# Kernel tuning notes

Hardware: AMD Instinct MI355X
Metric: run time of the kernel (lower is better)

The kernel has to match this reference:

```python
import jax, jax.numpy as jnp
import numpy as np
from jax import lax

LENGTH, WIDTH = 64, 64
INPUT_DIM = 1


def _convlstm_layer(x_tbchw, W, b):
    """Run one ConvLSTM layer over time. x_tbchw: (L,B,Cin,H,W).
    W: (4*hid, Cin+hid, 3, 3), b: (4*hid,). Returns (outputs (L,B,hid,H,W), last_h)."""
    L, B, _, H, Wd = x_tbchw.shape
    hid = W.shape[0] // 4
    h0 = jnp.zeros((B, hid, H, Wd), dtype=x_tbchw.dtype)
    c0 = jnp.zeros((B, hid, H, Wd), dtype=x_tbchw.dtype)

    def step(carry, xt):
        h, c = carry
        z = lax.conv_general_dilated(
            jnp.concatenate([xt, h], axis=1), W,
            window_strides=(1, 1), padding='SAME',
            dimension_numbers=('NCHW', 'OIHW', 'NCHW'))
        z = z + b[None, :, None, None]
        cc_i, cc_f, cc_o, cc_g = jnp.split(z, 4, axis=1)
        c_next = jax.nn.sigmoid(cc_f) * c + jax.nn.sigmoid(cc_i) * jnp.tanh(cc_g)
        h_next = jax.nn.sigmoid(cc_o) * jnp.tanh(c_next)
        return (h_next, c_next), h_next

    (h_last, _), outs = lax.scan(step, (h0, c0), x_tbchw)
    return outs, h_last


def setup_inputs() -> dict:
    key = jax.random.key(0)
    k1, k2, k3 = jax.random.split(key, 3)
    B, L, N = 16, 12, LENGTH * WIDTH
    emd, out_len = 128, 12
    return {
        'history_data': jax.random.normal(k1, (B, L, N, 1), dtype=jnp.float32),
        'future_data': jnp.zeros((B, L, N, 1), dtype=jnp.float32),
        'W0': jax.random.normal(k2, (4 * emd, INPUT_DIM + emd, 3, 3), dtype=jnp.float32) * 0.05,
        'b0': jnp.zeros((4 * emd,), dtype=jnp.float32),
        'W1': jax.random.normal(k3, (4 * out_len, emd + out_len, 3, 3), dtype=jnp.float32) * 0.05,
        'b1': jnp.zeros((4 * out_len,), dtype=jnp.float32),
        'batch_seen': 0,
        'epoch': 0,
        'train': 1,
    }


def reference(history_data, future_data, W0, b0, W1, b1, batch_seen, epoch, train):
    B, L, N, C = history_data.shape
    # (B,L,1,H,W) -> (L,B,1,H,W) for time-major scan
    x = history_data[..., :INPUT_DIM].reshape(B, L, INPUT_DIM, LENGTH, WIDTH)
    x = jnp.transpose(x, (1, 0, 2, 3, 4))
    outs0, _ = _convlstm_layer(x, W0, b0)          # (L,B,emd,H,W)
    _, h_last = _convlstm_layer(outs0, W1, b1)     # (B,out_len,H,W)
    prediction = h_last.reshape(B, L, LENGTH * WIDTH)[..., None]  # (B,L,N,1)
    return prediction
```

## Files before the change

### kernel.cpp

```cpp
#include <hip/hip_runtime.h>
#include <hip/hip_bf16.h>


typedef __attribute__((ext_vector_type(8))) short short8;
typedef __attribute__((ext_vector_type(4))) float float4v;

#define CS 160
#define KT0 1152
#define KTOT 1440
#define RSTR 2112
#define BSTR4 8448
#define BSTR6 12672

__device__ __forceinline__ float sigf(float x) { return 1.f / (1.f + __expf(-x)); }
__device__ __forceinline__ short f2hs(float v) {
  _Float16 h = (_Float16)v;
  return *(short*)&h;
}
__device__ __forceinline__ float bs2f(short s) {
  __hip_bfloat16 h; *(short*)&h = s; return __bfloat162float(h);
}
__device__ __forceinline__ short f2bs(float v) {
  __hip_bfloat16 h = __float2bfloat16(v);
  return *(short*)&h;
}

__device__ __forceinline__ void async_ld16(const short* g, short* l) {
  __builtin_amdgcn_global_load_lds(
      (const __attribute__((address_space(1))) unsigned int*)g,
      (__attribute__((address_space(3))) unsigned int*)l, 16, 0, 0);
}

__device__ __forceinline__ void stage_one4(const short* __restrict__ rowPtr, bool rowOK,
                                           short* dstRow, int lane,
                                           const short* __restrict__ zp, int j) {
  int e = j * 64 + lane;
  int px = e >> 2, v = e & 3;
  int xx = px - 1;
  bool ok = rowOK && (xx >= 0);
  const short* g = ok ? (rowPtr + (size_t)xx * CS + v * 8) : zp;
  async_ld16(g, dstRow + e * 8);
}

__device__ __forceinline__ void stage_row4(const short* __restrict__ rowPtr, bool rowOK,
                                           short* dstRow, int lane,
                                           const short* __restrict__ zp) {
  #pragma unroll
  for (int j = 0; j < 4; ++j) stage_one4(rowPtr, rowOK, dstRow, lane, zp, j);
}

__device__ __forceinline__ short8 tail_load(const short* __restrict__ srcChunk,
                                            bool rowOK, int lane) {
  short8 tv = {0, 0, 0, 0, 0, 0, 0, 0};
  if (lane < 4 && rowOK) tv = *(const short8*)(srcChunk + (size_t)63 * CS + lane * 8);
  return tv;
}

__device__ __forceinline__ void tail_write(short* dstRow, int lane, short8 tv) {
  if (lane < 8) {
    short8 w = {0, 0, 0, 0, 0, 0, 0, 0};
    if (lane < 4) w = tv;
    *(short8*)(dstRow + (64 + (lane >> 2)) * 32 + (lane & 3) * 8) = w;
  }
}

__global__ void detect_dtype(const unsigned short* __restrict__ w0, int* __restrict__ flag) {
  int lane = threadIdx.x;
  int cnt = 0;
  for (int i = 0; i < 4; ++i) {
    unsigned short u = w0[2 * (lane + 64 * i)];
    int e = (u >> 7) & 0xFF;
    unsigned long long b = __ballot(e >= 0xC0);
    cnt += __popcll(b);
  }
  if (lane == 0) *flag = (cnt > 32) ? 1 : 0;
}

__global__ void canon_b(const void* __restrict__ b0, const void* __restrict__ b1,
                        float* __restrict__ Bc0, float* __restrict__ Bc1,
                        const int* __restrict__ flag) {
  int i = blockIdx.x * 256 + threadIdx.x;
  int fl = *flag;
  if (i < 512) {
    float v = fl ? ((const float*)b0)[i] : bs2f(((const short*)b0)[i]);
    if (!isfinite(v) || fabsf(v) > 1e4f) v = 0.f;
    Bc0[i] = v;
  } else if (i < 560) {
    int j = i - 512;
    float v = fl ? ((const float*)b1)[j] : bs2f(((const short*)b1)[j]);
    if (!isfinite(v) || fabsf(v) > 1e4f) v = 0.f;
    Bc1[j] = v;
  }
}

__device__ __forceinline__ float ldw(const void* W, int idx, int fl) {
  float w = fl ? ((const float*)W)[idx] : bs2f(((const short*)W)[idx]);
  if (!isfinite(w) || fabsf(w) > 1e4f) w = 0.f;
  return w;
}

__global__ void prep_w0(const void* __restrict__ W0, short* __restrict__ Wp,
                        const int* __restrict__ flag) {
  int i = blockIdx.x * 256 + threadIdx.x;
  if (i >= 512 * KT0) return;
  int fl = *flag;
  int co = i / KT0, k = i - co * KT0;
  int tap = k >> 7, c = k & 127;
  Wp[i] = f2hs(ldw(W0, (co * 129 + 1 + c) * 9 + tap, fl));
}

__global__ void prep_wx(const void* __restrict__ W0, short* __restrict__ Wx,
                        const int* __restrict__ flag) {
  int i = blockIdx.x * 256 + threadIdx.x;
  if (i >= 512 * 16) return;
  int fl = *flag;
  int co = i >> 4, k = i & 15;
  float w = (k < 9) ? ldw(W0, (co * 129) * 9 + k, fl) : 0.f;
  Wx[i] = f2hs(w);
}

__global__ void prep_w1(const void* __restrict__ W1, short* __restrict__ Wp,
                        const int* __restrict__ flag) {
  int i = blockIdx.x * 256 + threadIdx.x;
  if (i >= 48 * KTOT) return;
  int fl = *flag;
  int co = i / KTOT, k = i - co * KTOT;
  int tap = k / CS, c = k - tap * CS;
  float w = (c < 140) ? ldw(W1, (co * 140 + c) * 9 + tap, fl) : 0.f;
  Wp[i] = f2hs(w);
}

__global__ void prep_xtap(const void* __restrict__ hist, short* __restrict__ Xtap,
                          const int* __restrict__ flag) {
  int i = blockIdx.x * 256 + threadIdx.x;
  int t = i >> 16, p = i & 65535;
  int b = p >> 12, pix = p & 4095, y = pix >> 6, x = pix & 63;
  int fl = *flag;
  short8 lo = {0, 0, 0, 0, 0, 0, 0, 0}, hi = {0, 0, 0, 0, 0, 0, 0, 0};
  #pragma unroll
  for (int k = 0; k < 9; ++k) {
    int dy = k / 3, dx = k - dy * 3;
    int yy = y + dy - 1, xx = x + dx - 1;
    float f = 0.f;
    if (yy >= 0 && yy < 64 && xx >= 0 && xx < 64) {
      int hidx = (b * 12 + t) * 4096 + yy * 64 + xx;
      f = fl ? ((const float*)hist)[hidx] : bs2f(((const short*)hist)[hidx]);
      if (!isfinite(f) || fabsf(f) > 1e4f) f = 0.f;
    }
    if (k < 8) lo[k] = f2hs(f); else hi[k - 8] = f2hs(f);
  }
  *(short8*)(Xtap + (size_t)i * 16) = lo;
  *(short8*)(Xtap + (size_t)i * 16 + 8) = hi;
}

__global__ __launch_bounds__(256, 2) void gemm_gate0(
    const short* __restrict__ Pcur, short* __restrict__ Pnext,
    const short* __restrict__ Wp, const short* __restrict__ Wx,
    const float* __restrict__ Bc0, float* __restrict__ C0,
    const short* __restrict__ Xtap, const short* __restrict__ zp, int t) {
  int pbx = blockIdx.x;
  int xcd = pbx & 7, i = pbx >> 3;
  int mt = xcd * 32 + (i & 31);
  int nt = i >> 5;
  int b = mt >> 4, y0 = (mt & 15) * 4;
  int tid = threadIdx.x, wave = tid >> 6, lane = tid & 63;
  int ln15 = lane & 15, quad = lane >> 4;
  int wm = wave & 1, wn = wave >> 1;
  int hc = nt * 32 + wn * 16 + ln15;

  __shared__ __align__(16) short halo[2 * BSTR6];

  float4v acc[8][4];
  #pragma unroll
  for (int i2 = 0; i2 < 8; ++i2)
    #pragma unroll
    for (int j = 0; j < 4; ++j) acc[i2][j] = (float4v){0.f, 0.f, 0.f, 0.f};

  const short* wbase = Wp + (size_t)hc * KT0 + quad * 8;
  short8 bcur[4], bnxt[4];
  #pragma unroll
  for (int g = 0; g < 4; ++g)
    bcur[g] = *(const short8*)(wbase + (size_t)g * 128 * KT0);

  int yyA = y0 - 1 + wave;
  bool okA = (yyA >= 0) && (yyA < 64);
  const short* baseA = Pcur + (size_t)((b * 64 + yyA) * 64) * CS;
  int yyB = y0 + 3 + wave;
  bool okB = (wave < 2) && (yyB < 64);
  const short* baseB = Pcur + (size_t)((b * 64 + yyB) * 64) * CS;

  bool hiQ = quad >= 2;
  short8 ax[8], bxr[4];
  #pragma unroll
  for (int mf = 0; mf < 8; ++mf) {
    int row = y0 + wm * 2 + (mf >> 2);
    int pixB = (b * 64 + row) * 64 + (mf & 3) * 16 + ln15;
    ax[mf] = *(const short8*)(Xtap + ((size_t)t * 65536 + pixB) * 16 + (quad & 1) * 8);
  }
  #pragma unroll
  for (int g = 0; g < 4; ++g) {
    const short* wxp = Wx + (size_t)(g * 128 + hc) * 16 + (quad & 1) * 8;
    bxr[g] = *(const short8*)(hiQ ? zp : wxp);
  }
  short8 tA = tail_load(baseA, okA, lane);
  short8 tB = tail_load(baseB, okB, lane);

  stage_row4(baseA, okA, halo + wave * RSTR, lane, zp);
  if (wave < 2) stage_row4(baseB, okB, halo + (4 + wave) * RSTR, lane, zp);

  #pragma unroll
  for (int g = 0; g < 4; ++g)
    #pragma unroll
    for (int mf = 0; mf < 8; ++mf)
      acc[mf][g] = __builtin_amdgcn_mfma_f32_16x16x32_f16(ax[mf], bxr[g], acc[mf][g], 0, 0, 0);

  tail_write(halo + wave * RSTR, lane, tA);
  if (wave < 2) tail_write(halo + (4 + wave) * RSTR, lane, tB);
  __syncthreads();

  for (int ch = 0; ch < 4; ++ch) {
    int c0 = ch * 32;
    const short* cur = halo + (ch & 1) * BSTR6;
    short* nd = halo + ((ch + 1) & 1) * BSTR6;
    const short* srcA = baseA + c0 + 32;
    const short* srcB = baseB + c0 + 32;
    short8 nA = {0, 0, 0, 0, 0, 0, 0, 0}, nB = {0, 0, 0, 0, 0, 0, 0, 0};
    if (ch < 3) {
      nA = tail_load(srcA, okA, lane);
      if (wave < 2) nB = tail_load(srcB, okB, lane);
    }
    #pragma unroll
    for (int tap = 0; tap < 9; ++tap) {
      int dy = tap / 3, dx = tap - dy * 3;
      if (ch < 3 && tap < 4) {
        stage_one4(srcA, okA, nd + wave * RSTR, lane, zp, tap);
        if (wave < 2) stage_one4(srcB, okB, nd + (4 + wave) * RSTR, lane, zp, tap);
      }
      int ntap = (tap < 8) ? tap + 1 : 0;
      int nc0 = (tap < 8) ? c0 : ((ch < 3) ? c0 + 32 : c0);
      #pragma unroll
      for (int g = 0; g < 4; ++g)
        bnxt[g] = *(const short8*)(wbase + (size_t)g * 128 * KT0 + ntap * 128 + nc0);

      short8 af[8];
      #pragma unroll
      for (int mf = 0; mf < 8; ++mf)
        af[mf] = *(const short8*)&cur[(wm * 2 + (mf >> 2) + dy) * RSTR
                                      + ((mf & 3) * 16 + ln15 + dx) * 32 + quad * 8];
      #pragma unroll
      for (int g = 0; g < 4; ++g)
        #pragma unroll
        for (int mf = 0; mf < 8; ++mf)
          acc[mf][g] = __builtin_amdgcn_mfma_f32_16x16x32_f16(af[mf], bcur[g], acc[mf][g], 0, 0, 0);
      #pragma unroll
      for (int g = 0; g < 4; ++g) bcur[g] = bnxt[g];
    }
    if (ch < 3) {
      tail_write(nd + wave * RSTR, lane, nA);
      if (wave < 2) tail_write(nd + (4 + wave) * RSTR, lane, nB);
    }
    __syncthreads();
  }

  float bi = Bc0[hc], bff = Bc0[128 + hc], bo = Bc0[256 + hc], bg = Bc0[384 + hc];
  #pragma unroll
  for (int mf = 0; mf < 8; ++mf) {
    int row = y0 + wm * 2 + (mf >> 2);
    int pixRow = (b * 64 + row) * 64;
    #pragma unroll
    for (int r = 0; r < 4; ++r) {
      int x = (mf & 3) * 16 + quad * 4 + r;
      int pix = pixRow + x;
      float zi = acc[mf][0][r] + bi;
      float zf = acc[mf][1][r] + bff;
      float zo = acc[mf][2][r] + bo;
      float zg = acc[mf][3][r] + bg;
      float cprev = C0[(size_t)pix * 128 + hc];
      float cn = sigf(zf) * cprev + sigf(zi) * tanhf(zg);
      float hn = sigf(zo) * tanhf(cn);
      C0[(size_t)pix * 128 + hc] = cn;
      Pnext[(size_t)pix * CS + hc] = f2hs(hn);
    }
  }
}

__global__ __launch_bounds__(256, 4) void gemm_gate1(
    const short* __restrict__ Prd, short* __restrict__ Pwr,
    const short* __restrict__ Wp, const float* __restrict__ Bc1,
    float* __restrict__ C1, void* __restrict__ outp,
    const short* __restrict__ zp, const int* __restrict__ flagp, int t) {
  int pbx = blockIdx.x;
  int bid = (pbx & 7) * 64 + (pbx >> 3);
  int b = bid >> 5, y0 = (bid & 31) * 2;
  int tid = threadIdx.x, wave = tid >> 6, lane = tid & 63;
  int ln15 = lane & 15, quad = lane >> 4;
  int wr = wave >> 1, wh = wave & 1;
  int flagv = *flagp;

  __shared__ __align__(16) short halo[2 * BSTR4];

  float4v acc[2][3];
  #pragma unroll
  for (int i = 0; i < 2; ++i)
    #pragma unroll
    for (int j = 0; j < 3; ++j) acc[i][j] = (float4v){0.f, 0.f, 0.f, 0.f};

  int yy = y0 - 1 + wave;
  bool rowOK = (yy >= 0) && (yy < 64);
  const short* rowBase = Prd + (size_t)((b * 64 + yy) * 64) * CS;

  const short* wbase = Wp + (size_t)ln15 * KTOT + quad * 8;
  short8 bcur[3], bnxt[3];
  #pragma unroll
  for (int nf = 0; nf < 3; ++nf)
    bcur[nf] = *(const short8*)(wbase + (size_t)nf * 16 * KTOT);

  short8 tP = tail_load(rowBase, rowOK, lane);
  stage_row4(rowBase, rowOK, halo + wave * RSTR, lane, zp);
  tail_write(halo + wave * RSTR, lane, tP);
  __syncthreads();

  for (int ch = 0; ch < 5; ++ch) {
    int c0 = ch * 32;
    const short* cur = halo + (ch & 1) * BSTR4;
    short* nxtDst = halo + ((ch + 1) & 1) * BSTR4 + wave * RSTR;
    const short* nxtSrc = rowBase + c0 + 32;
    short8 nP = {0, 0, 0, 0, 0, 0, 0, 0};
    if (ch < 4) nP = tail_load(nxtSrc, rowOK, lane);
    #pragma unroll
    for (int tap = 0; tap < 9; ++tap) {
      int dy = tap / 3, dx = tap - dy * 3;
      if (ch < 4 && tap < 4)
        stage_one4(nxtSrc, rowOK, nxtDst, lane, zp, tap);
      int ntap = (tap < 8) ? tap + 1 : 0;
      int nc0 = (tap < 8) ? c0 : ((ch < 4) ? c0 + 32 : c0);
      #pragma unroll
      for (int nf = 0; nf < 3; ++nf)
        bnxt[nf] = *(const short8*)(wbase + (size_t)nf * 16 * KTOT + ntap * CS + nc0);

      short8 af[2];
      #pragma unroll
      for (int mf = 0; mf < 2; ++mf)
        af[mf] = *(const short8*)&cur[(wr + dy) * RSTR + (wh * 32 + mf * 16 + ln15 + dx) * 32
                                      + quad * 8];
      #pragma unroll
      for (int nf = 0; nf < 3; ++nf)
        #pragma unroll
        for (int mf = 0; mf < 2; ++mf)
          acc[mf][nf] = __builtin_amdgcn_mfma_f32_16x16x32_f16(af[mf], bcur[nf], acc[mf][nf], 0, 0, 0);
      #pragma unroll
      for (int nf = 0; nf < 3; ++nf) bcur[nf] = bnxt[nf];
    }
    if (ch < 4) tail_write(nxtDst, lane, nP);
    __syncthreads();
  }

  float* zbuf = (float*)halo;
  #pragma unroll
  for (int mf = 0; mf < 2; ++mf)
    #pragma unroll
    for (int nf = 0; nf < 3; ++nf)
      #pragma unroll
      for (int r = 0; r < 4; ++r) {
        int pxl = wr * 64 + wh * 32 + mf * 16 + quad * 4 + r;
        zbuf[pxl * 48 + nf * 16 + ln15] = acc[mf][nf][r];
      }
  __syncthreads();

  #pragma unroll
  for (int k = 0; k < 6; ++k) {
    int id = k * 256 + tid;
    int hc = id >> 7, pxl = id & 127;
    float zi = zbuf[pxl * 48 + hc]      + Bc1[hc];
    float zf = zbuf[pxl * 48 + 12 + hc] + Bc1[12 + hc];
    float zo = zbuf[pxl * 48 + 24 + hc] + Bc1[24 + hc];
    float zg = zbuf[pxl * 48 + 36 + hc] + Bc1[36 + hc];
    int y = y0 + (pxl >> 6), x = pxl & 63;
    int pix = (b * 64 + y) * 64 + x;
    float cprev = C1[(size_t)pix * 12 + hc];
    float cn = sigf(zf) * cprev + sigf(zi) * tanhf(zg);
    float hn = sigf(zo) * tanhf(cn);
    C1[(size_t)pix * 12 + hc] = cn;
    Pwr[(size_t)pix * CS + 128 + hc] = f2hs(hn);
    if (t == 11) {
      int oidx = (b * 12 + hc) * 4096 + y * 64 + x;
      if (flagv) ((float*)outp)[oidx] = hn;
      else ((short*)outp)[oidx] = f2bs(hn);
    }
  }
}

extern "C" void kernel_launch(void* const* d_in, const int* in_sizes, int n_in,
                              void* d_out, int out_size, void* d_ws, size_t ws_size,
                              hipStream_t stream) {
  const void* hist = d_in[0];
  const void* W0 = d_in[2];
  const void* b0 = d_in[3];
  const void* W1 = d_in[4];
  const void* b1 = d_in[5];

  char* ws = (char*)d_ws;
  const size_t PszB = (size_t)16 * 4096 * CS * 2;
  short* P[2] = {(short*)ws, (short*)(ws + PszB)};
  float* C0 = (float*)(ws + 2 * PszB);
  const size_t C0e = 2 * PszB + 33554432;
  float* C1 = (float*)(ws + C0e);
  const size_t C1e = C0e + 3145728;
  short* zp = (short*)(ws + C1e);
  const size_t zpe = C1e + 256;
  short* Xtap = (short*)(ws + zpe);
  const size_t Xte = zpe + (size_t)12 * 65536 * 16 * 2;
  short* Wp0 = (short*)(ws + Xte);
  const size_t W0e = Xte + (size_t)512 * KT0 * 2;
  short* Wx0 = (short*)(ws + W0e);
  const size_t Wxe = W0e + 512 * 16 * 2;
  short* Wp1 = (short*)(ws + Wxe);
  const size_t W1e = Wxe + (size_t)48 * KTOT * 2;
  float* Bc0 = (float*)(ws + W1e);
  float* Bc1 = (float*)(ws + W1e + 2048);
  int* flag = (int*)(ws + W1e + 2048 + 192);

  hipMemsetAsync(ws, 0, zpe, stream);
  detect_dtype<<<1, 64, 0, stream>>>((const unsigned short*)W0, flag);
  canon_b<<<3, 256, 0, stream>>>(b0, b1, Bc0, Bc1, flag);
  prep_w0<<<(512 * KT0 + 255) / 256, 256, 0, stream>>>(W0, Wp0, flag);
  prep_wx<<<32, 256, 0, stream>>>(W0, Wx0, flag);
  prep_w1<<<(48 * KTOT + 255) / 256, 256, 0, stream>>>(W1, Wp1, flag);
  prep_xtap<<<3072, 256, 0, stream>>>(hist, Xtap, flag);

  for (int t = 0; t < 12; ++t) {
    gemm_gate0<<<1024, 256, 0, stream>>>(P[t & 1], P[(t + 1) & 1], Wp0, Wx0, Bc0, C0,
                                         Xtap, zp, t);
    gemm_gate1<<<512, 256, 0, stream>>>(P[(t + 1) & 1], P[t & 1], Wp1, Bc1, C1,
                                        d_out, zp, flag, t);
  }
}
```

Before: 1.899 ms.

## Split gate1 GEMM taps across wave pairs with LDS reduction

Changes gemm_gate1's work split from a 2x2 pixel tiling across waves to a split-K scheme. Each wave pair covers a full 64-pixel row, and the two pairs alternate 3x3 taps by parity, so every wave loads four A fragments and reuses each B fragment across them. The partial accumulators are then summed through LDS in two phases with an extra barrier. This halves redundant B-weight loads per MFMA, at the cost of more accumulator registers (launch bounds lowered to 2 blocks), uneven tap counts per chunk, and an added reduction pass.

```diff
diff --git a/kernel.cpp b/kernel.cpp
--- a/kernel.cpp
+++ b/kernel.cpp
@@ -284,7 +284,7 @@
   }
 }
 
-__global__ __launch_bounds__(256, 4) void gemm_gate1(
+__global__ __launch_bounds__(256, 2) void gemm_gate1(
     const short* __restrict__ Prd, short* __restrict__ Pwr,
     const short* __restrict__ Wp, const float* __restrict__ Bc1,
     float* __restrict__ C1, void* __restrict__ outp,
@@ -294,14 +294,14 @@
   int b = bid >> 5, y0 = (bid & 31) * 2;
   int tid = threadIdx.x, wave = tid >> 6, lane = tid & 63;
   int ln15 = lane & 15, quad = lane >> 4;
-  int wr = wave >> 1, wh = wave & 1;
+  int w = wave & 1, kp = wave >> 1;
   int flagv = *flagp;
 
   __shared__ __align__(16) short halo[2 * BSTR4];
 
-  float4v acc[2][3];
-  #pragma unroll
-  for (int i = 0; i < 2; ++i)
+  float4v acc[4][3];
+  #pragma unroll
+  for (int i = 0; i < 4; ++i)
     #pragma unroll
     for (int j = 0; j < 3; ++j) acc[i][j] = (float4v){0.f, 0.f, 0.f, 0.f};
 
@@ -310,10 +310,10 @@
   const short* rowBase = Prd + (size_t)((b * 64 + yy) * 64) * CS;
 
   const short* wbase = Wp + (size_t)ln15 * KTOT + quad * 8;
-  short8 bcur[3], bnxt[3];
+  short8 bcur[3];
   #pragma unroll
   for (int nf = 0; nf < 3; ++nf)
-    bcur[nf] = *(const short8*)(wbase + (size_t)nf * 16 * KTOT);
+    bcur[nf] = *(const short8*)(wbase + (size_t)nf * 16 * KTOT + kp * CS);
 
   short8 tP = tail_load(rowBase, rowOK, lane);
   stage_row4(rowBase, rowOK, halo + wave * RSTR, lane, zp);
@@ -327,44 +327,63 @@
     const short* nxtSrc = rowBase + c0 + 32;
     short8 nP = {0, 0, 0, 0, 0, 0, 0, 0};
     if (ch < 4) nP = tail_load(nxtSrc, rowOK, lane);
-    #pragma unroll
-    for (int tap = 0; tap < 9; ++tap) {
-      int dy = tap / 3, dx = tap - dy * 3;
-      if (ch < 4 && tap < 4)
-        stage_one4(nxtSrc, rowOK, nxtDst, lane, zp, tap);
-      int ntap = (tap < 8) ? tap + 1 : 0;
-      int nc0 = (tap < 8) ? c0 : ((ch < 4) ? c0 + 32 : c0);
-      #pragma unroll
-      for (int nf = 0; nf < 3; ++nf)
-        bnxt[nf] = *(const short8*)(wbase + (size_t)nf * 16 * KTOT + ntap * CS + nc0);
-
-      short8 af[2];
-      #pragma unroll
-      for (int mf = 0; mf < 2; ++mf)
-        af[mf] = *(const short8*)&cur[(wr + dy) * RSTR + (wh * 32 + mf * 16 + ln15 + dx) * 32
-                                      + quad * 8];
-      #pragma unroll
-      for (int nf = 0; nf < 3; ++nf)
-        #pragma unroll
-        for (int mf = 0; mf < 2; ++mf)
-          acc[mf][nf] = __builtin_amdgcn_mfma_f32_16x16x32_f16(af[mf], bcur[nf], acc[mf][nf], 0, 0, 0);
-      #pragma unroll
-      for (int nf = 0; nf < 3; ++nf) bcur[nf] = bnxt[nf];
+    int ts = (kp + ch * 9) & 1;
+    #pragma unroll
+    for (int tt = 0; tt < 5; ++tt) {
+      int tap = ts + tt * 2;
+      if (tap <= 8) {
+        int dy = tap / 3, dx = tap - dy * 3;
+        if (ch < 4 && tt < 4)
+          stage_one4(nxtSrc, rowOK, nxtDst, lane, zp, tt);
+        int ntap = tap + 2, nc0 = c0;
+        if (ntap > 8) { ntap -= 9; nc0 = (ch < 4) ? c0 + 32 : c0; }
+        short8 bnxt[3];
+        #pragma unroll
+        for (int nf = 0; nf < 3; ++nf)
+          bnxt[nf] = *(const short8*)(wbase + (size_t)nf * 16 * KTOT + ntap * CS + nc0);
+
+        short8 af[4];
+        #pragma unroll
+        for (int mf = 0; mf < 4; ++mf)
+          af[mf] = *(const short8*)&cur[(w + dy) * RSTR + (mf * 16 + ln15 + dx) * 32
+                                        + quad * 8];
+        #pragma unroll
+        for (int nf = 0; nf < 3; ++nf)
+          #pragma unroll
+          for (int mf = 0; mf < 4; ++mf)
+            acc[mf][nf] = __builtin_amdgcn_mfma_f32_16x16x32_f16(af[mf], bcur[nf], acc[mf][nf], 0, 0, 0);
+        #pragma unroll
+        for (int nf = 0; nf < 3; ++nf) bcur[nf] = bnxt[nf];
+      }
     }
     if (ch < 4) tail_write(nxtDst, lane, nP);
     __syncthreads();
   }
 
   float* zbuf = (float*)halo;
-  #pragma unroll
-  for (int mf = 0; mf < 2; ++mf)
-    #pragma unroll
-    for (int nf = 0; nf < 3; ++nf)
-      #pragma unroll
-      for (int r = 0; r < 4; ++r) {
-        int pxl = wr * 64 + wh * 32 + mf * 16 + quad * 4 + r;
-        zbuf[pxl * 48 + nf * 16 + ln15] = acc[mf][nf][r];
-      }
+  if (kp == 0) {
+    #pragma unroll
+    for (int mf = 0; mf < 4; ++mf)
+      #pragma unroll
+      for (int nf = 0; nf < 3; ++nf)
+        #pragma unroll
+        for (int r = 0; r < 4; ++r) {
+          int pxl = w * 64 + mf * 16 + quad * 4 + r;
+          zbuf[pxl * 48 + nf * 16 + ln15] = acc[mf][nf][r];
+        }
+  }
+  __syncthreads();
+  if (kp == 1) {
+    #pragma unroll
+    for (int mf = 0; mf < 4; ++mf)
+      #pragma unroll
+      for (int nf = 0; nf < 3; ++nf)
+        #pragma unroll
+        for (int r = 0; r < 4; ++r) {
+          int pxl = w * 64 + mf * 16 + quad * 4 + r;
+          zbuf[pxl * 48 + nf * 16 + ln15] += acc[mf][nf][r];
+        }
+  }
   __syncthreads();
 
   #pragma unroll
```

Result: faster. 1.814 ms (median of 2 runs) (-4.5%).
